# Kernel optimization log

Measured on AMD Instinct MI355X. Metric: run time of the kernel, lower is better.

The kernel has to match this reference:

```python
import jax, jax.numpy as jnp
import numpy as np

FEAT_STRIDE = 16
NUM_ANCHORS = 9
PRE_NMS_TOPN = 6000
POST_NMS_TOPN = 300
NMS_THRESH = 0.7
ANCHOR_SCALES = np.array([8.0, 16.0, 32.0])
ANCHOR_RATIOS = np.array([0.5, 1.0, 2.0])
BBOX_CLIP = float(np.log(1000.0 / 16.0))  # standard delta clip to avoid exp overflow


def _mkanchors(ws, hs, xc, yc):
    return np.stack([xc - 0.5 * (ws - 1), yc - 0.5 * (hs - 1),
                     xc + 0.5 * (ws - 1), yc + 0.5 * (hs - 1)], axis=1)


def _base_anchors(base_size=16):
    w = h = float(base_size)
    xc = yc = 0.5 * (base_size - 1)
    size = w * h
    ws = np.round(np.sqrt(size / ANCHOR_RATIOS))
    hs = np.round(ws * ANCHOR_RATIOS)
    ratio_anchors = _mkanchors(ws, hs, xc, yc)
    out = []
    for a in ratio_anchors:
        aw = a[2] - a[0] + 1.0
        ah = a[3] - a[1] + 1.0
        axc = a[0] + 0.5 * (aw - 1.0)
        ayc = a[1] + 0.5 * (ah - 1.0)
        out.append(_mkanchors(aw * ANCHOR_SCALES, ah * ANCHOR_SCALES, axc, ayc))
    return np.concatenate(out, axis=0)  # [A, 4]


def _all_anchors(H, W):
    base = _base_anchors(FEAT_STRIDE)
    sx = np.arange(W) * FEAT_STRIDE
    sy = np.arange(H) * FEAT_STRIDE
    shift_x, shift_y = np.meshgrid(sx, sy)  # row-major over (h, w)
    shifts = np.stack([shift_x.ravel(), shift_y.ravel(),
                       shift_x.ravel(), shift_y.ravel()], axis=1)
    return (shifts[:, None, :] + base[None, :, :]).reshape(-1, 4).astype(np.float32)


def _conv2d(x, w, b, pad):
    y = jax.lax.conv_general_dilated(x, w, (1, 1), [(pad, pad), (pad, pad)],
                                     dimension_numbers=("NCHW", "OIHW", "NCHW"))
    return y + b[None, :, None, None]


def _decode_clip(anchors, deltas, im_h, im_w):
    aw = anchors[:, 2] - anchors[:, 0] + 1.0
    ah = anchors[:, 3] - anchors[:, 1] + 1.0
    acx = anchors[:, 0] + 0.5 * aw
    acy = anchors[:, 1] + 0.5 * ah
    dx, dy = deltas[:, 0], deltas[:, 1]
    dw = jnp.clip(deltas[:, 2], -BBOX_CLIP, BBOX_CLIP)
    dh = jnp.clip(deltas[:, 3], -BBOX_CLIP, BBOX_CLIP)
    pcx = dx * aw + acx
    pcy = dy * ah + acy
    pw = jnp.exp(dw) * aw
    ph = jnp.exp(dh) * ah
    x1 = jnp.clip(pcx - 0.5 * pw, 0.0, im_w - 1.0)
    y1 = jnp.clip(pcy - 0.5 * ph, 0.0, im_h - 1.0)
    x2 = jnp.clip(pcx + 0.5 * pw, 0.0, im_w - 1.0)
    y2 = jnp.clip(pcy + 0.5 * ph, 0.0, im_h - 1.0)
    return jnp.stack([x1, y1, x2, y2], axis=1)


def _nms_suppressed(boxes, thresh):
    # boxes sorted by score descending; greedy NMS, returns bool suppression mask
    n = boxes.shape[0]
    idx = jnp.arange(n)
    areas = (boxes[:, 2] - boxes[:, 0] + 1.0) * (boxes[:, 3] - boxes[:, 1] + 1.0)
    def body(i, supp):
        b = boxes[i]
        iw = jnp.maximum(0.0, jnp.minimum(b[2], boxes[:, 2]) - jnp.maximum(b[0], boxes[:, 0]) + 1.0)
        ih = jnp.maximum(0.0, jnp.minimum(b[3], boxes[:, 3]) - jnp.maximum(b[1], boxes[:, 1]) + 1.0)
        inter = iw * ih
        iou = inter / (areas[i] + areas - inter)
        kill = (~supp[i]) & (iou > thresh) & (idx > i)
        return supp | kill
    return jax.lax.fori_loop(0, n, body, jnp.zeros((n,), jnp.bool_))


def reference(feature, im_info, w_rpn_conv, b_rpn_conv, w_score, b_score, w_bbox, b_bbox):
    N, C, H, W = feature.shape
    A = NUM_ANCHORS
    rpn_feat = _conv2d(feature, w_rpn_conv, b_rpn_conv, 1)             # [N,512,H,W]
    cls_logits = _conv2d(rpn_feat, w_score, b_score, 0)                # [N,2A,H,W]
    # _reshape_layer(x,2) + softmax(dim=1) + _reshape_layer(x,2A): channels [0:A]=bg, [A:2A]=fg
    fg_prob = jax.nn.softmax(cls_logits.reshape(N, 2, A, H, W), axis=1)[:, 1]  # [N,A,H,W]
    scores = fg_prob.transpose(0, 2, 3, 1).reshape(-1)                 # (h,w,a) order, matches anchors
    deltas = _conv2d(rpn_feat, w_bbox, b_bbox, 0).transpose(0, 2, 3, 1).reshape(-1, 4)
    anchors = jnp.asarray(_all_anchors(H, W))                          # [H*W*A, 4]
    im_h = im_info[0].astype(jnp.float32)
    im_w = im_info[1].astype(jnp.float32)
    proposals = _decode_clip(anchors, deltas, im_h, im_w)
    top_scores, order = jax.lax.top_k(scores, PRE_NMS_TOPN)            # sorted desc
    boxes = proposals[order]
    supp = _nms_suppressed(jax.lax.stop_gradient(boxes), NMS_THRESH)
    masked = jnp.where(supp, -1.0, jax.lax.stop_gradient(top_scores))
    _, keep = jax.lax.top_k(masked, POST_NMS_TOPN)                     # first POST_NMS survivors
    rois_boxes = boxes[keep]                                           # [300, 4]
    roi_scores = top_scores[keep][:, None]                             # [300, 1]
    rois = jnp.concatenate([jnp.zeros((POST_NMS_TOPN, 1), rois_boxes.dtype), rois_boxes], axis=1)
    return rois, roi_scores, feature


def setup_inputs() -> dict:
    key = jax.random.key(0)
    ks = jax.random.split(key, 4)
    C, H, W, A = 512, 128, 128, NUM_ANCHORS
    feature = jax.random.normal(ks[0], (1, C, H, W), jnp.float32)
    w_rpn_conv = jax.random.normal(ks[1], (512, C, 3, 3), jnp.float32) * 0.01
    b_rpn_conv = jnp.zeros((512,), jnp.float32)
    w_score = jax.random.normal(ks[2], (2 * A, 512, 1, 1), jnp.float32) * 0.01
    b_score = jnp.zeros((2 * A,), jnp.float32)
    w_bbox = jax.random.normal(ks[3], (4 * A, 512, 1, 1), jnp.float32) * 0.001
    b_bbox = jnp.zeros((4 * A,), jnp.float32)
    im_info = jnp.array([H * FEAT_STRIDE, W * FEAT_STRIDE, 1], jnp.int32)
    return {"feature": feature, "im_info": im_info,
            "w_rpn_conv": w_rpn_conv, "b_rpn_conv": b_rpn_conv,
            "w_score": w_score, "b_score": b_score,
            "w_bbox": w_bbox, "b_bbox": b_bbox}
```

## Files before the change

kernel.cpp:

```cpp
#include <hip/hip_runtime.h>
#include <hip/hip_bf16.h>


#define HH 128
#define WW 128
#define HW 16384
#define CC 512
#define NANCH 9
#define NTOT 147456
#define PRE_TOPN 6000
#define POST_TOPN 300
#define NMS_WORDS 94
#define CAND_CAP 16384

typedef unsigned int u32;
typedef unsigned long long u64;

__constant__ float c_anch[9][4] = {
  { -84.f,  -40.f,  99.f,  55.f},
  {-176.f,  -88.f, 191.f, 103.f},
  {-360.f, -184.f, 375.f, 199.f},
  { -56.f,  -56.f,  71.f,  71.f},
  {-120.f, -120.f, 135.f, 135.f},
  {-248.f, -248.f, 263.f, 263.f},
  { -36.f,  -80.f,  51.f,  95.f},
  { -80.f, -168.f,  95.f, 183.f},
  {-168.f, -344.f, 183.f, 351.f}
};

__global__ __launch_bounds__(256)
void wcvt(const float* __restrict__ wconv, double* __restrict__ wd)
{
  int idx = blockIdx.x * 256 + threadIdx.x;
  int t  = idx % 9;
  int ic = (idx / 9) & 511;
  int oc = idx / 4608;
  int g  = oc >> 3, o8 = oc & 7;
  wd[(size_t)g * 36864 + ic * 72 + t * 8 + o8] = (double)wconv[idx];
}

__global__ __launch_bounds__(512)
void conv3x3(const float* __restrict__ feat, const double* __restrict__ wd,
             const float* __restrict__ bias, float* __restrict__ out)
{
  __shared__ double sA[4][3][162];
  const int tid = threadIdx.x;
  const int oc0 = (blockIdx.x & 7) << 6;
  const int r   = blockIdx.x >> 3;
  const int wv  = __builtin_amdgcn_readfirstlane(tid >> 6);
  const int l   = tid & 63;

  const int c0 = 2 * l;
  const int x0 = c0 + (c0 >> 2);
  const int x1 = (c0 + 1) + ((c0 + 1) >> 2);
  const int x2 = (c0 + 2) + ((c0 + 2) >> 2);
  const int x3 = (c0 + 3) + ((c0 + 3) >> 2);

  if (tid < 24) {
    int ic = tid / 6, rm = tid % 6;
    sA[ic][rm >> 1][(rm & 1) ? 161 : 0] = 0.0;
  }

  double acc[8][2];
  #pragma unroll
  for (int o = 0; o < 8; ++o) {
    double bv = (double)bias[oc0 + wv * 8 + o];
    acc[o][0] = bv; acc[o][1] = bv;
  }

  const double* wg = wd + (size_t)((oc0 >> 3) + wv) * 36864;

  for (int ic0 = 0; ic0 < CC; ic0 += 4) {
    __syncthreads();
    if (tid < 384) {
      int icr = tid >> 5;
      int ic = icr / 3, rr = icr % 3;
      int lam = tid & 31;
      int grow = r - 1 + rr;
      float4 v = make_float4(0.f, 0.f, 0.f, 0.f);
      if (grow >= 0 && grow < HH)
        v = *reinterpret_cast<const float4*>(
              &feat[(ic0 + ic) * HW + grow * WW + lam * 4]);
      double* dst = &sA[ic][rr][5 * lam];
      dst[1] = (double)v.x;
      dst[2] = (double)v.y;
      dst[3] = (double)v.z;
      dst[5] = (double)v.w;
    }
    __syncthreads();

    const double* wc = wg + ic0 * 72;
    #pragma unroll
    for (int ic = 0; ic < 4; ++ic) {
      #pragma unroll
      for (int ky = 0; ky < 3; ++ky) {
        const double* arow = sA[ic][ky];
        double a0 = arow[x0], a1 = arow[x1], a2 = arow[x2], a3 = arow[x3];
        const double* wp = wc + ic * 72 + ky * 24;
        #pragma unroll
        for (int kx = 0; kx < 3; ++kx) {
          double b0 = (kx == 0) ? a0 : ((kx == 1) ? a1 : a2);
          double b1 = (kx == 0) ? a1 : ((kx == 1) ? a2 : a3);
          #pragma unroll
          for (int o = 0; o < 8; ++o) {
            double w = wp[kx * 8 + o];
            acc[o][0] = fma(b0, w, acc[o][0]);
            acc[o][1] = fma(b1, w, acc[o][1]);
          }
        }
      }
    }
  }

  #pragma unroll
  for (int o = 0; o < 8; ++o) {
    float2 v;
    v.x = (float)acc[o][0];
    v.y = (float)acc[o][1];
    *reinterpret_cast<float2*>(
      &out[(size_t)(oc0 + wv * 8 + o) * HW + r * WW + 2 * l]) = v;
  }
}

__global__ __launch_bounds__(256, 4)
void conv3x3_fb(const float* __restrict__ feat, const float* __restrict__ wconv,
                const float* __restrict__ bias, float* __restrict__ out)
{
  __shared__ float sA[8][3][136];
  __shared__ float sW[72][64];
  const int tid  = threadIdx.x;
  const int oc0  = (blockIdx.x & 7) << 6;
  const int r    = blockIdx.x >> 3;
  const int ocg  = tid >> 4;
  const int p    = tid & 15;

  if (tid < 48) {
    int ic = tid / 6, rm = tid % 6;
    sA[ic][rm >> 1][(rm & 1) ? 132 : 3] = 0.f;
  }

  double acc[4][8];
  #pragma unroll
  for (int o = 0; o < 4; ++o) {
    double bv = (double)bias[oc0 + ocg * 4 + o];
    #pragma unroll
    for (int j = 0; j < 8; ++j) acc[o][j] = bv;
  }

  for (int ic0 = 0; ic0 < CC; ic0 += 8) {
    __syncthreads();
    #pragma unroll
    for (int k = 0; k < 3; ++k) {
      int s   = tid + 256 * k;
      int icr = s >> 5;
      int ic  = icr / 3, rr = icr % 3;
      int c4  = (s & 31) << 2;
      int grow = r - 1 + rr;
      float4 v = make_float4(0.f, 0.f, 0.f, 0.f);
      if (grow >= 0 && grow < HH)
        v = *reinterpret_cast<const float4*>(&feat[(ic0 + ic) * HW + grow * WW + c4]);
      *reinterpret_cast<float4*>(&sA[ic][rr][4 + c4]) = v;
    }
    {
      int oc = tid & 63, part = tid >> 6;
      const float* wp = &wconv[(size_t)((oc0 + oc) * CC + ic0) * 9 + part * 18];
      #pragma unroll
      for (int k = 0; k < 18; ++k) sW[part * 18 + k][oc] = wp[k];
    }
    __syncthreads();

    for (int ic = 0; ic < 8; ++ic) {
      #pragma unroll
      for (int ky = 0; ky < 3; ++ky) {
        double w[3][4];
        #pragma unroll
        for (int kx = 0; kx < 3; ++kx)
          #pragma unroll
          for (int o = 0; o < 4; ++o)
            w[kx][o] = (double)sW[ic * 9 + ky * 3 + kx][ocg * 4 + o];
        const float* arow = &sA[ic][ky][4];
        #pragma unroll
        for (int j = 0; j < 8; ++j) {
          int c = p + 16 * j;
          double a0 = (double)arow[c - 1];
          double a1 = (double)arow[c];
          double a2 = (double)arow[c + 1];
          #pragma unroll
          for (int o = 0; o < 4; ++o) {
            acc[o][j] = fma(a0, w[0][o], acc[o][j]);
            acc[o][j] = fma(a1, w[1][o], acc[o][j]);
            acc[o][j] = fma(a2, w[2][o], acc[o][j]);
          }
        }
      }
    }
  }

  #pragma unroll
  for (int o = 0; o < 4; ++o) {
    float* op = &out[(size_t)(oc0 + ocg * 4 + o) * HW + r * WW];
    #pragma unroll
    for (int j = 0; j < 8; ++j)
      op[p + 16 * j] = (float)acc[o][j];
  }
}

__global__ __launch_bounds__(256, 2)
void conv1x1_decode(const float* __restrict__ rfeat, const float* __restrict__ wsc,
                    const float* __restrict__ bsc, const float* __restrict__ wbb,
                    const float* __restrict__ bbb, const int* __restrict__ im_info,
                    float* __restrict__ scores, double4* __restrict__ props,
                    u32* __restrict__ hist)
{
  __shared__ float  sA[32][64];
  __shared__ float  sW[32][56];
  __shared__ double sOut[64][56];
  const int tid  = threadIdx.x;
  const int px0  = blockIdx.x * 64;
  const int q    = tid >> 6;
  const int px_l = tid & 63;
  const int o0   = q * 14;

  double acc[14];
  #pragma unroll
  for (int o = 0; o < 14; ++o) {
    int oo = o0 + o;
    float b = 0.f;
    if (oo < 18) b = bsc[oo];
    else if (oo < 54) b = bbb[oo - 18];
    acc[o] = (double)b;
  }

  for (int ic0 = 0; ic0 < CC; ic0 += 32) {
    __syncthreads();
    #pragma unroll
    for (int k = 0; k < 2; ++k) {
      int s  = tid + 256 * k;
      int ic = s >> 4;
      int c4 = (s & 15) << 2;
      *reinterpret_cast<float4*>(&sA[ic][c4]) =
        *reinterpret_cast<const float4*>(&rfeat[(ic0 + ic) * HW + px0 + c4]);
    }
    for (int idx = tid; idx < 32 * 56; idx += 256) {
      int ic = idx / 56, o = idx % 56;
      float v = 0.f;
      if (o < 18) v = wsc[o * CC + ic0 + ic];
      else if (o < 54) v = wbb[(o - 18) * CC + ic0 + ic];
      sW[ic][o] = v;
    }
    __syncthreads();
    for (int ic = 0; ic < 32; ++ic) {
      double a = (double)sA[ic][px_l];
      #pragma unroll
      for (int o = 0; o < 14; ++o)
        acc[o] = fma(a, (double)sW[ic][o0 + o], acc[o]);
    }
  }
  #pragma unroll
  for (int o = 0; o < 14; ++o) sOut[px_l][o0 + o] = acc[o];
  __syncthreads();

  const double im_h = (double)im_info[0];
  const double im_w = (double)im_info[1];
  const double BCLIP = 4.1351665567423557;
  for (int t = tid; t < 64 * NANCH; t += 256) {
    int pl = t / 9, a = t % 9;
    int gp = px0 + pl;
    double l0 = sOut[pl][a], l1 = sOut[pl][9 + a];
    double sc = 1.0 / (1.0 + exp(l0 - l1));
    float scf = (float)sc;
    int gi = gp * 9 + a;
    scores[gi] = scf;
    atomicAdd(&hist[__float_as_uint(scf) >> 16], 1u);

    double dx = sOut[pl][18 + 4 * a + 0];
    double dy = sOut[pl][18 + 4 * a + 1];
    double dw = sOut[pl][18 + 4 * a + 2];
    double dh = sOut[pl][18 + 4 * a + 3];
    int wq = gp & 127, hq = gp >> 7;
    double ax1 = (double)c_anch[a][0] + 16.0 * wq;
    double ay1 = (double)c_anch[a][1] + 16.0 * hq;
    double ax2 = (double)c_anch[a][2] + 16.0 * wq;
    double ay2 = (double)c_anch[a][3] + 16.0 * hq;
    double aw = ax2 - ax1 + 1.0, ah = ay2 - ay1 + 1.0;
    double acx = ax1 + 0.5 * aw,  acy = ay1 + 0.5 * ah;
    dw = fmin(fmax(dw, -BCLIP), BCLIP);
    dh = fmin(fmax(dh, -BCLIP), BCLIP);
    double pcx = dx * aw + acx, pcy = dy * ah + acy;
    double pw = exp(dw) * aw,   ph = exp(dh) * ah;
    double x1 = fmin(fmax(pcx - 0.5 * pw, 0.0), im_w - 1.0);
    double y1 = fmin(fmax(pcy - 0.5 * ph, 0.0), im_h - 1.0);
    double x2 = fmin(fmax(pcx + 0.5 * pw, 0.0), im_w - 1.0);
    double y2 = fmin(fmax(pcy + 0.5 * ph, 0.0), im_h - 1.0);
    props[gi] = make_double4(x1, y1, x2, y2);
  }
}

__global__ __launch_bounds__(1024)
void scan_hist(const u32* __restrict__ hist, u32* __restrict__ scal)
{
  __shared__ u32 suf[1024];
  const int t = threadIdx.x;
  u32 s = 0;
  for (int k = 0; k < 64; ++k) s += hist[t * 64 + k];
  suf[t] = s;
  __syncthreads();
  for (int off = 1; off < 1024; off <<= 1) {
    u32 v = (t + off < 1024) ? suf[t + off] : 0u;
    __syncthreads();
    suf[t] += v;
    __syncthreads();
  }
  u32 here = suf[t];
  u32 next = (t < 1023) ? suf[t + 1] : 0u;
  if (here >= PRE_TOPN && (t == 1023 || next < PRE_TOPN)) {
    u32 cum = next;
    int T = t * 64;
    for (int b = 63; b >= 0; --b) {
      cum += hist[t * 64 + b];
      if (cum >= PRE_TOPN) { T = t * 64 + b; break; }
    }
    scal[1] = (u32)T;
  }
}

__global__ void compact_cand(const float* __restrict__ scores,
                             u32* __restrict__ scal, u64* __restrict__ cand)
{
  int t = blockIdx.x * 256 + threadIdx.x;
  if (t >= NTOT) return;
  u32 bits = __float_as_uint(scores[t]);
  if ((bits >> 16) >= scal[1]) {
    u32 pos = atomicAdd(&scal[0], 1u);
    if (pos < CAND_CAP)
      cand[pos] = ((u64)bits << 32) | (u64)(0xFFFFFFFFu - (u32)t);
  }
}

__global__ __launch_bounds__(1024)
void sort_topk(const u64* __restrict__ cand, const u32* __restrict__ scal,
               const double4* __restrict__ props, float* __restrict__ tscore,
               double4* __restrict__ boxes)
{
  __shared__ u64 sk[CAND_CAP];
  u32 n = scal[0]; if (n > CAND_CAP) n = CAND_CAP;
  const int SZ = (n <= 8192) ? 8192 : CAND_CAP;
  for (int t = threadIdx.x; t < SZ; t += 1024)
    sk[t] = (t < (int)n) ? cand[t] : 0ull;
  __syncthreads();
  for (int k = 2; k <= SZ; k <<= 1)
    for (int j = k >> 1; j > 0; j >>= 1) {
      for (int t = threadIdx.x; t < SZ; t += 1024) {
        int p = t ^ j;
        if (p > t) {
          u64 va = sk[t], vb = sk[p];
          bool sw = ((t & k) == 0) ? (va < vb) : (va > vb);
          if (sw) { sk[t] = vb; sk[p] = va; }
        }
      }
      __syncthreads();
    }
  for (int t = threadIdx.x; t < PRE_TOPN; t += 1024) {
    u64 key = sk[t];
    u32 idx = 0xFFFFFFFFu - (u32)key;
    tscore[t] = __uint_as_float((u32)(key >> 32));
    boxes[t]  = props[idx];
  }
}

__global__ __launch_bounds__(64)
void nms_mask(const double4* __restrict__ boxes, u64* __restrict__ mask)
{
  const int bi = blockIdx.y, bj = blockIdx.x;
  const int t = threadIdx.x;
  const int i = bi * 64 + t;
  if (bj < bi) { if (i < PRE_TOPN) mask[(u32)i * NMS_WORDS + bj] = 0ull; return; }
  __shared__ double4 cb[64];
  __shared__ double  ca[64];
  const int j0 = bj * 64;
  if (j0 + t < PRE_TOPN) {
    double4 b = boxes[j0 + t];
    cb[t] = b;
    ca[t] = (b.z - b.x + 1.0) * (b.w - b.y + 1.0);
  }
  __syncthreads();
  if (i >= PRE_TOPN) return;
  double4 bb = boxes[i];
  double ai = (bb.z - bb.x + 1.0) * (bb.w - bb.y + 1.0);
  const int jmax = min(64, PRE_TOPN - j0);
  u64 word = 0ull;
  for (int jj = 0; jj < jmax; ++jj) {
    int j = j0 + jj;
    if (j <= i) continue;
    double4 cj = cb[jj];
    double iw = fmin(bb.z, cj.z) - fmax(bb.x, cj.x) + 1.0;
    double ih = fmin(bb.w, cj.w) - fmax(bb.y, cj.y) + 1.0;
    iw = fmax(iw, 0.0); ih = fmax(ih, 0.0);
    double inter = iw * ih;
    double iou = inter / (ai + ca[jj] - inter);
    if (iou > 0.7) word |= (1ull << jj);
  }
  mask[(u32)i * NMS_WORDS + bj] = word;
}

__global__ __launch_bounds__(256)
void nms_finalize(const u64* __restrict__ mask, const double4* __restrict__ boxes,
                  const float* __restrict__ tscore, float* __restrict__ out)
{
  __shared__ u64 rem[NMS_WORDS];
  __shared__ u64 alv[NMS_WORDS];
  __shared__ int rows[68];
  __shared__ int nrows;
  __shared__ int pre[NMS_WORDS + 1];
  __shared__ int keep[POST_TOPN];
  const int tid = threadIdx.x;
  if (tid < NMS_WORDS) rem[tid] = 0ull;
  __syncthreads();

  for (int c = 0; c < NMS_WORDS; ++c) {
    if (tid < 64) {
      int row = c * 64 + tid;
      u64 m = (row < PRE_TOPN) ? mask[(u32)row * NMS_WORDS + c] : 0ull;
      u64 cur = rem[c];
      for (int b = 0; b < 64; ++b) {
        u64 mb = (u64)__shfl((long long)m, b, 64);
        if (!((cur >> b) & 1ull)) cur |= mb;
      }
      if (tid == 0) {
        rem[c] = cur;
        u64 valid = (c == NMS_WORDS - 1) ? ((1ull << 48) - 1ull) : ~0ull;
        alv[c] = (~cur) & valid;
      }
    }
    if (tid == 255) nrows = 0;
    __syncthreads();
    if (tid < 64 && ((alv[c] >> tid) & 1ull))
      rows[atomicAdd(&nrows, 1)] = c * 64 + tid;
    __syncthreads();
    const int nr = nrows;
    if (tid < 4 && nr > 0) rows[nr + tid] = rows[0];
    __syncthreads();
    if (nr > 0) {
      int w = c + 1 + (tid >> 1);
      if (w < NMS_WORDS) {
        const int sl = tid & 1;
        const int G = (nr + 3) >> 2;
        u64 acc = 0ull;
        for (int g = sl; g < G; g += 2) {
          int b = g << 2;
          int r0 = rows[b], r1 = rows[b + 1], r2 = rows[b + 2], r3 = rows[b + 3];
          acc |= mask[(u32)r0 * NMS_WORDS + w] | mask[(u32)r1 * NMS_WORDS + w]
               | mask[(u32)r2 * NMS_WORDS + w] | mask[(u32)r3 * NMS_WORDS + w];
        }
        if (acc) atomicOr((unsigned long long*)&rem[w], (unsigned long long)acc);
      }
    }
    __syncthreads();
  }

  if (tid == 0) {
    int s = 0;
    for (int c = 0; c < NMS_WORDS; ++c) { pre[c] = s; s += __popcll(alv[c]); }
    pre[NMS_WORDS] = s;
  }
  __syncthreads();
  const int total = pre[NMS_WORDS];
  if (tid < NMS_WORDS) {
    int p = pre[tid];
    u64 bits = alv[tid];
    while (bits && p < POST_TOPN) {
      int b = __ffsll(bits) - 1;
      bits &= bits - 1;
      keep[p] = tid * 64 + b;
      ++p;
    }
  }
  __syncthreads();
  if (total < POST_TOPN) {
    if (tid == 0) {
      int p = total;
      for (int c = 0; c < NMS_WORDS && p < POST_TOPN; ++c) {
        u64 valid = (c == NMS_WORDS - 1) ? ((1ull << 48) - 1ull) : ~0ull;
        u64 bits = rem[c] & valid;
        while (bits && p < POST_TOPN) {
          int b = __ffsll(bits) - 1;
          bits &= bits - 1;
          keep[p++] = c * 64 + b;
        }
      }
    }
    __syncthreads();
  }

  for (int t = tid; t < POST_TOPN; t += 256) {
    int r = keep[t];
    double4 b = boxes[r];
    out[t * 5 + 0] = 0.f;
    out[t * 5 + 1] = (float)b.x;
    out[t * 5 + 2] = (float)b.y;
    out[t * 5 + 3] = (float)b.z;
    out[t * 5 + 4] = (float)b.w;
    out[POST_TOPN * 5 + t] = tscore[r];
  }
}

extern "C" void kernel_launch(void* const* d_in, const int* in_sizes, int n_in,
                              void* d_out, int out_size, void* d_ws, size_t ws_size,
                              hipStream_t stream)
{
  const float* feature = (const float*)d_in[0];
  const int*   im_info = (const int*)d_in[1];
  const float* w_conv  = (const float*)d_in[2];
  const float* b_conv  = (const float*)d_in[3];
  const float* w_sc    = (const float*)d_in[4];
  const float* b_sc    = (const float*)d_in[5];
  const float* w_bb    = (const float*)d_in[6];
  const float* b_bb    = (const float*)d_in[7];
  float* out = (float*)d_out;

  char* ws = (char*)d_ws;
  float*   rfeat  = (float*)(ws);
  double*  wd     = (double*)(ws + 33554432);
  float*   scores = (float*)(ws + 33554432);
  double4* props  = (double4*)(ws + 34144256);
  u64*     mask   = (u64*)(ws + 34144256);
  u32*     hist   = (u32*)(ws + 38862848);
  u32*     scal   = (u32*)(ws + 39124992);
  u64*     cand   = (u64*)(ws + 39125248);
  float*   tscore = (float*)(ws + 39256320);
  double4* boxes  = (double4*)(ws + 39280384);

  const bool big = (ws_size >= 52428800ull);
  if (big) {
    wcvt<<<9216, 256, 0, stream>>>(w_conv, wd);
    conv3x3<<<1024, 512, 0, stream>>>(feature, wd, b_conv, rfeat);
  } else {
    conv3x3_fb<<<1024, 256, 0, stream>>>(feature, w_conv, b_conv, rfeat);
  }

  hipMemsetAsync(hist, 0, 65536 * sizeof(u32), stream);
  hipMemsetAsync(scal, 0, 256, stream);

  conv1x1_decode<<<256, 256, 0, stream>>>(rfeat, w_sc, b_sc, w_bb, b_bb, im_info,
                                          scores, props, hist);
  scan_hist<<<1, 1024, 0, stream>>>(hist, scal);
  compact_cand<<<(NTOT + 255) / 256, 256, 0, stream>>>(scores, scal, cand);
  sort_topk<<<1, 1024, 0, stream>>>(cand, scal, props, tscore, boxes);
  nms_mask<<<dim3(NMS_WORDS, NMS_WORDS), 64, 0, stream>>>(boxes, mask);
  nms_finalize<<<1, 256, 0, stream>>>(mask, boxes, tscore, out);

  hipMemcpyAsync(out + POST_TOPN * 6, feature, (size_t)CC * HW * sizeof(float),
                 hipMemcpyDeviceToDevice, stream);
}
```

Before: 2.815 ms.

## Split conv LDS tile into even/odd planes, stage 8 channels; simplify NMS sweep

```diff
diff --git a/kernel.cpp b/kernel.cpp
--- a/kernel.cpp
+++ b/kernel.cpp
@@ -43,22 +43,18 @@
 void conv3x3(const float* __restrict__ feat, const double* __restrict__ wd,
              const float* __restrict__ bias, float* __restrict__ out)
 {
-  __shared__ double sA[4][3][162];
+  __shared__ double sAe[8][3][66];
+  __shared__ double sAo[8][3][66];
   const int tid = threadIdx.x;
   const int oc0 = (blockIdx.x & 7) << 6;
   const int r   = blockIdx.x >> 3;
   const int wv  = __builtin_amdgcn_readfirstlane(tid >> 6);
   const int l   = tid & 63;
 
-  const int c0 = 2 * l;
-  const int x0 = c0 + (c0 >> 2);
-  const int x1 = (c0 + 1) + ((c0 + 1) >> 2);
-  const int x2 = (c0 + 2) + ((c0 + 2) >> 2);
-  const int x3 = (c0 + 3) + ((c0 + 3) >> 2);
-
-  if (tid < 24) {
+  if (tid < 48) {
     int ic = tid / 6, rm = tid % 6;
-    sA[ic][rm >> 1][(rm & 1) ? 161 : 0] = 0.0;
+    if (rm & 1) sAo[ic][rm >> 1][64] = 0.0;
+    else        sAe[ic][rm >> 1][0]  = 0.0;
   }
 
   double acc[8][2];
@@ -70,32 +66,37 @@
 
   const double* wg = wd + (size_t)((oc0 >> 3) + wv) * 36864;
 
-  for (int ic0 = 0; ic0 < CC; ic0 += 4) {
-    __syncthreads();
-    if (tid < 384) {
-      int icr = tid >> 5;
-      int ic = icr / 3, rr = icr % 3;
-      int lam = tid & 31;
-      int grow = r - 1 + rr;
-      float4 v = make_float4(0.f, 0.f, 0.f, 0.f);
-      if (grow >= 0 && grow < HH)
-        v = *reinterpret_cast<const float4*>(
-              &feat[(ic0 + ic) * HW + grow * WW + lam * 4]);
-      double* dst = &sA[ic][rr][5 * lam];
-      dst[1] = (double)v.x;
-      dst[2] = (double)v.y;
-      dst[3] = (double)v.z;
-      dst[5] = (double)v.w;
+  for (int ic0 = 0; ic0 < CC; ic0 += 8) {
+    __syncthreads();
+    #pragma unroll
+    for (int k = 0; k < 2; ++k) {
+      int s = tid + 512 * k;
+      if (s < 768) {
+        int icr = s >> 5;
+        int ic = icr / 3, rr = icr % 3;
+        int lam = s & 31;
+        int grow = r - 1 + rr;
+        float4 v = make_float4(0.f, 0.f, 0.f, 0.f);
+        if (grow >= 0 && grow < HH)
+          v = *reinterpret_cast<const float4*>(
+                &feat[(ic0 + ic) * HW + grow * WW + lam * 4]);
+        sAo[ic][rr][2 * lam]     = (double)v.x;
+        sAe[ic][rr][2 * lam + 1] = (double)v.y;
+        sAo[ic][rr][2 * lam + 1] = (double)v.z;
+        sAe[ic][rr][2 * lam + 2] = (double)v.w;
+      }
     }
     __syncthreads();
 
     const double* wc = wg + ic0 * 72;
     #pragma unroll
-    for (int ic = 0; ic < 4; ++ic) {
+    for (int ic = 0; ic < 8; ++ic) {
       #pragma unroll
       for (int ky = 0; ky < 3; ++ky) {
-        const double* arow = sA[ic][ky];
-        double a0 = arow[x0], a1 = arow[x1], a2 = arow[x2], a3 = arow[x3];
+        double a0 = sAe[ic][ky][l];
+        double a1 = sAo[ic][ky][l];
+        double a2 = sAe[ic][ky][l + 1];
+        double a3 = sAo[ic][ky][l + 1];
         const double* wp = wc + ic * 72 + ky * 24;
         #pragma unroll
         for (int kx = 0; kx < 3; ++kx) {
@@ -409,7 +410,7 @@
 {
   __shared__ u64 rem[NMS_WORDS];
   __shared__ u64 alv[NMS_WORDS];
-  __shared__ int rows[68];
+  __shared__ int rows[72];
   __shared__ int nrows;
   __shared__ int pre[NMS_WORDS + 1];
   __shared__ int keep[POST_TOPN];
@@ -438,21 +439,25 @@
       rows[atomicAdd(&nrows, 1)] = c * 64 + tid;
     __syncthreads();
     const int nr = nrows;
-    if (tid < 4 && nr > 0) rows[nr + tid] = rows[0];
+    if (tid < 8 && nr > 0) rows[nr + tid] = rows[0];
     __syncthreads();
     if (nr > 0) {
-      int w = c + 1 + (tid >> 1);
+      int w = c + 1 + tid;
       if (w < NMS_WORDS) {
-        const int sl = tid & 1;
-        const int G = (nr + 3) >> 2;
+        const int G = (nr + 7) >> 3;
         u64 acc = 0ull;
-        for (int g = sl; g < G; g += 2) {
-          int b = g << 2;
-          int r0 = rows[b], r1 = rows[b + 1], r2 = rows[b + 2], r3 = rows[b + 3];
-          acc |= mask[(u32)r0 * NMS_WORDS + w] | mask[(u32)r1 * NMS_WORDS + w]
-               | mask[(u32)r2 * NMS_WORDS + w] | mask[(u32)r3 * NMS_WORDS + w];
+        for (int g = 0; g < G; ++g) {
+          int b = g << 3;
+          acc |= mask[(u32)rows[b]     * NMS_WORDS + w]
+               | mask[(u32)rows[b + 1] * NMS_WORDS + w]
+               | mask[(u32)rows[b + 2] * NMS_WORDS + w]
+               | mask[(u32)rows[b + 3] * NMS_WORDS + w]
+               | mask[(u32)rows[b + 4] * NMS_WORDS + w]
+               | mask[(u32)rows[b + 5] * NMS_WORDS + w]
+               | mask[(u32)rows[b + 6] * NMS_WORDS + w]
+               | mask[(u32)rows[b + 7] * NMS_WORDS + w];
         }
-        if (acc) atomicOr((unsigned long long*)&rem[w], (unsigned long long)acc);
+        rem[w] |= acc;
       }
     }
     __syncthreads();
```

Result: slower. 3.575 ms (+27.0%).
